# Kernel tuning notes

Measured on AMD Instinct MI355X. Metric: run time of the kernel, lower is better.

## Reference

```python
import jax, jax.numpy as jnp
import numpy as np
import math

B, S, D = 2, 2048, 2048
H, KVH, WIN = 16, 4, 256
HD = D // H            # 128
QPER = H // KVH        # 4


def setup_inputs() -> dict:
    key = jax.random.key(0)
    ks = jax.random.split(key, 9)
    s = lambda k, shp: jax.random.normal(k, shp, dtype=jnp.float32) * 0.02
    return {
        "x": jax.random.normal(ks[0], (B, S, D), dtype=jnp.float32),
        "Wq": s(ks[1], (D, D)),            "bq": jnp.zeros((D,), jnp.float32),
        "Wk": s(ks[2], (D, KVH * HD)),      "bk": jnp.zeros((KVH * HD,), jnp.float32),
        "Wv": s(ks[3], (D, KVH * HD)),      "bv": jnp.zeros((KVH * HD,), jnp.float32),
        "Wo": s(ks[4], (D, D)),            "bo": jnp.zeros((D,), jnp.float32),
    }


def reference(x, Wq, bq, Wk, bk, Wv, bv, Wo, bo):
    b, s, _ = x.shape
    # projections
    Q = (x @ Wq + bq).reshape(b, s, H, HD).transpose(0, 2, 1, 3)     # [b,H,s,hd]
    K = (x @ Wk + bk).reshape(b, s, KVH, HD).transpose(0, 2, 1, 3)   # [b,kvh,s,hd]
    V = (x @ Wv + bv).reshape(b, s, KVH, HD).transpose(0, 2, 1, 3)   # [b,kvh,s,hd]
    # GQA grouping: head h = g*QPER + q
    Qg = Q.reshape(b, KVH, QPER, s, HD)                               # [b,g,q,s,hd]
    scores = jnp.einsum('bgqsd,bgtd->bgqst', Qg, K)                   # [b,g,q,s,s]
    i = jnp.arange(s)[:, None]
    j = jnp.arange(s)[None, :]
    keep = (j <= i) & (j >= i - WIN + 1)                              # [s,s]
    scores = jnp.where(keep, scores, -jnp.inf)
    A = jax.nn.softmax(scores / math.sqrt(HD), axis=-1)
    O = jnp.einsum('bgqst,bgtd->bgqsd', A, V)                         # [b,g,q,s,hd]
    O = O.reshape(b, H, s, HD).transpose(0, 2, 1, 3).reshape(b, s, D)
    return O @ Wo + bo
```

## Files before the change

### kernel.cpp

```cpp
#include <hip/hip_runtime.h>
#include <hip/hip_bf16.h>
#include <math.h>

typedef __bf16 bf16_t;
typedef bf16_t bf16x8 __attribute__((ext_vector_type(8)));
typedef bf16_t bf16x4 __attribute__((ext_vector_type(4)));
typedef float  f32x4  __attribute__((ext_vector_type(4)));

#define NB    2
#define SEQ   2048
#define DIM   2048
#define NHEAD 16
#define NKVH  4
#define HDIM  128
#define WINSZ 256
#define KVD   512
#define QKVN  3072
#define MROWS 4096

__device__ __forceinline__ void async_copy16(const void* g, void* lds) {
    __builtin_amdgcn_global_load_lds(
        (const __attribute__((address_space(1))) void*)g,
        (__attribute__((address_space(3))) void*)lds,
        16, 0, 0);
}

__global__ __launch_bounds__(256) void cvt_f32_bf16(const float* __restrict__ in,
                                                    bf16_t* __restrict__ out, int n) {
    int i = (blockIdx.x * 256 + threadIdx.x) * 4;
    if (i >= n) return;
    float4 v = *(const float4*)(in + i);
    bf16x4 o;
    o[0] = (bf16_t)v.x; o[1] = (bf16_t)v.y; o[2] = (bf16_t)v.z; o[3] = (bf16_t)v.w;
    *(bf16x4*)(out + i) = o;
}

__global__ __launch_bounds__(256) void transpose_cvt(const float* __restrict__ in,
                                                     bf16_t* __restrict__ out, int K, int N) {
    __shared__ float tile[32][33];
    int tx = threadIdx.x & 31, ty = threadIdx.x >> 5;
    int n0 = blockIdx.x * 32, k0 = blockIdx.y * 32;
    for (int r = ty; r < 32; r += 8)
        tile[r][tx] = in[(size_t)(k0 + r) * N + n0 + tx];
    __syncthreads();
    for (int r = ty; r < 32; r += 8)
        out[(size_t)(n0 + r) * K + k0 + tx] = (bf16_t)tile[tx][r];
}

__global__ __launch_bounds__(256) void concat_bias(const float* __restrict__ bq,
                                                   const float* __restrict__ bk,
                                                   const float* __restrict__ bv,
                                                   float* __restrict__ out) {
    int i = blockIdx.x * 256 + threadIdx.x;
    if (i >= QKVN) return;
    float v = (i < DIM) ? bq[i] : ((i < DIM + KVD) ? bk[i - DIM] : bv[i - DIM - KVD]);
    out[i] = v;
}

__global__ __launch_bounds__(256) void transpose_v(const bf16_t* __restrict__ QKV,
                                                   bf16_t* __restrict__ Vtb) {
    __shared__ bf16_t t[32][33];
    int tx = threadIdx.x & 31, ty = threadIdx.x >> 5;
    int jb = blockIdx.x, c0 = blockIdx.y * 32, b = blockIdx.z;
    int j0 = jb * 32;
    for (int r = ty; r < 32; r += 8)
        t[r][tx] = QKV[((size_t)(b * SEQ) + j0 + r) * QKVN + (DIM + KVD) + c0 + tx];
    __syncthreads();
    int g = c0 >> 7, dl = c0 & 127;
    bf16_t* outb = Vtb + (((size_t)(b * NKVH) + g) * 64 + jb) * 4096;
    for (int r = ty; r < 32; r += 8)
        outb[(dl + r) * 32 + tx] = t[tx][r];
}

template <int BM, int BN, typename OutT>
__global__ __launch_bounds__(512, 1) void gemm8p(const bf16_t* __restrict__ A,
                                                 const bf16_t* __restrict__ Bt,
                                                 const float* __restrict__ bias,
                                                 OutT* __restrict__ C,
                                                 int M, int N, int K, float qs, int qcols) {
    constexpr int AISS = BM / 128;
    constexpr int BISS = BN / 128;
    constexpr int ISS  = AISS + BISS;
    constexpr int MF   = BM / 32;
    constexpr int NF   = BN / 64;
    constexpr int AHALF = BM * 32;
    constexpr int BHALF = BN * 32;
    constexpr int BUFSZ = 2 * (AHALF + BHALF);
    __shared__ bf16_t lds[2 * BUFSZ];

    const int tid  = threadIdx.x;
    const int wave = tid >> 6;
    const int lane = tid & 63;
    const int lg = lane >> 4, lc = lane & 15;
    const int wr = wave >> 2, wc = wave & 3;

    const int nbn  = N / BN;
    const int nblk = (M / BM) * nbn;
    const int qq   = nblk >> 3;
    const int swz  = (blockIdx.x & 7) * qq + (blockIdx.x >> 3);
    const long brow = (long)(swz / nbn) * BM;
    const long bcol = (long)(swz % nbn) * BN;

    const int srow   = tid >> 2;
    const int schunk = (tid & 3) ^ ((tid >> 3) & 3);

    f32x4 acc[MF][NF] = {};

    auto stage = [&](int buf, int p, int kt) {
        const int kcol = kt * 64 + p * 32 + schunk * 8;
        const bf16_t* gA = A + (brow + srow) * (long)K + kcol;
        bf16_t* dA = lds + buf * BUFSZ + p * AHALF + tid * 8;
#pragma unroll
        for (int i = 0; i < AISS; ++i)
            async_copy16(gA + (long)i * 128 * K, dA + i * 4096);
        const bf16_t* gB = Bt + (bcol + srow) * (long)K + kcol;
        bf16_t* dB = lds + buf * BUFSZ + 2 * AHALF + p * BHALF + tid * 8;
#pragma unroll
        for (int i = 0; i < BISS; ++i)
            async_copy16(gB + (long)i * 128 * K, dB + i * 4096);
    };

    stage(0, 0, 0);
    stage(0, 1, 0);

    const int NT = K >> 6;
    const int cswz = (lg ^ ((lc >> 1) & 3)) * 8;
    for (int t = 0; t < NT; ++t) {
#pragma unroll
        for (int p = 0; p < 2; ++p) {
            if (t == NT - 1 && p == 1) {
                asm volatile("s_waitcnt vmcnt(0)" ::: "memory");
            } else if constexpr (ISS == 4) {
                asm volatile("s_waitcnt vmcnt(4)" ::: "memory");
            } else {
                asm volatile("s_waitcnt vmcnt(3)" ::: "memory");
            }
            __builtin_amdgcn_s_barrier();
            asm volatile("" ::: "memory");
            const bf16_t* Ab = lds + (t & 1) * BUFSZ + p * AHALF;
            const bf16_t* Bb = lds + (t & 1) * BUFSZ + 2 * AHALF + p * BHALF;
            bf16x8 af[MF], bv[NF];
#pragma unroll
            for (int m = 0; m < MF; ++m)
                af[m] = *(const bf16x8*)(Ab + (wr * (BM / 2) + m * 16 + lc) * 32 + cswz);
#pragma unroll
            for (int n = 0; n < NF; ++n)
                bv[n] = *(const bf16x8*)(Bb + (wc * 64 + n * 16 + lc) * 32 + cswz);
            if (t + 1 < NT) stage((t + 1) & 1, p, t + 1);
            asm volatile("s_waitcnt lgkmcnt(0)" ::: "memory");
            __builtin_amdgcn_sched_barrier(0);
            __builtin_amdgcn_s_setprio(1);
#pragma unroll
            for (int m = 0; m < MF; ++m)
#pragma unroll
                for (int n = 0; n < NF; ++n)
                    acc[m][n] = __builtin_amdgcn_mfma_f32_16x16x32_bf16(af[m], bv[n], acc[m][n], 0, 0, 0);
            __builtin_amdgcn_s_setprio(0);
        }
    }

#pragma unroll
    for (int n = 0; n < NF; ++n) {
        int gc = (int)bcol + wc * 64 + n * 16 + lc;
        float bvs = bias[gc];
        bool ds = gc < qcols;
#pragma unroll
        for (int m = 0; m < MF; ++m) {
            long gr = brow + wr * (BM / 2) + m * 16 + 4 * lg;
#pragma unroll
            for (int r = 0; r < 4; ++r) {
                float v = acc[m][n][r] + bvs;
                if (ds) v *= qs;
                C[(gr + r) * (long)N + gc] = (OutT)v;
            }
        }
    }
}

__global__ __launch_bounds__(256) void attn_kernel(const bf16_t* __restrict__ QKV,
                                                   const bf16_t* __restrict__ Vtb,
                                                   bf16_t* __restrict__ Ob) {
    __shared__ bf16_t Kls[2][32 * 128];
    __shared__ bf16_t Vls[2][128 * 32];
    __shared__ bf16_t Pls[4][16 * 40];

    const int wv   = threadIdx.x >> 6;
    const int lane = threadIdx.x & 63;
    const int lg = lane >> 4, lc = lane & 15;

    const int swb = (blockIdx.x & 7) * 128 + (blockIdx.x >> 3);
    const int ti = swb & 127;
    const int g  = (swb >> 7) & 3;
    const int b  = swb >> 9;
    const int h  = g * 4 + wv;
    const int i0 = ti * 16;
    const int irow = i0 + lc;
    bf16_t* P = &Pls[wv][0];

    bf16x8 qf[4];
    {
        const bf16_t* qp = QKV + ((size_t)(b * SEQ) + irow) * QKVN + h * HDIM + lg * 8;
#pragma unroll
        for (int kk = 0; kk < 4; ++kk) qf[kk] = *(const bf16x8*)(qp + kk * 32);
    }

    auto stage = [&](int buf, int jb) {
        const int j0s = jb * 32;
        const bf16_t* kgb = QKV + ((size_t)(b * SEQ) + j0s) * QKVN + DIM + g * HDIM;
#pragma unroll
        for (int ii = 0; ii < 2; ++ii) {
            int i = wv * 2 + ii;
            int row = i * 4 + (lane >> 4);
            int ch  = (lane & 15) ^ (row & 7);
            async_copy16(kgb + (size_t)row * QKVN + ch * 8, &Kls[buf][i * 512]);
        }
        const bf16_t* vgb = Vtb + (((size_t)(b * NKVH) + g) * 64 + jb) * 4096;
#pragma unroll
        for (int ii = 0; ii < 2; ++ii) {
            int i = wv * 2 + ii;
            int row = i * 16 + (lane >> 2);
            int ch  = (lane & 3) ^ ((row ^ (row >> 2)) & 3);
            async_copy16(vgb + row * 32 + ch * 8, &Vls[buf][i * 512]);
        }
    };

    float m_run = -1e30f, l_run = 0.f;
    f32x4 oacc[8] = {};

    int jlo = i0 - (WINSZ - 1); if (jlo < 0) jlo = 0;
    const int jb0 = jlo >> 5;
    const int jb1 = (i0 + 15) >> 5;

    stage(0, jb0);

    for (int jb = jb0; jb <= jb1; ++jb) {
        const int j0 = jb * 32;
        const int cur = (jb - jb0) & 1;
        asm volatile("s_waitcnt vmcnt(0)" ::: "memory");
        __builtin_amdgcn_s_barrier();
        asm volatile("" ::: "memory");

        bf16x8 kf[2][4];
#pragma unroll
        for (int t = 0; t < 2; ++t)
#pragma unroll
            for (int kk = 0; kk < 4; ++kk) {
                int row = t * 16 + lc;
                int ch  = (kk * 4 + lg) ^ (row & 7);
                kf[t][kk] = *(const bf16x8*)(&Kls[cur][row * 128 + ch * 8]);
            }
        if (jb < jb1) stage(cur ^ 1, jb + 1);
        asm volatile("s_waitcnt lgkmcnt(0)" ::: "memory");
        __builtin_amdgcn_sched_barrier(0);

        f32x4 s[2];
        __builtin_amdgcn_s_setprio(1);
#pragma unroll
        for (int t = 0; t < 2; ++t) {
            f32x4 sv = {};
#pragma unroll
            for (int kk = 0; kk < 4; ++kk)
                sv = __builtin_amdgcn_mfma_f32_16x16x32_bf16(kf[t][kk], qf[kk], sv, 0, 0, 0);
            s[t] = sv;
        }
        __builtin_amdgcn_s_setprio(0);

        const bool edge = (j0 < i0 - 240) || (j0 > i0 - 31);
        if (edge) {
#pragma unroll
            for (int t = 0; t < 2; ++t)
#pragma unroll
                for (int r = 0; r < 4; ++r) {
                    int j = j0 + t * 16 + 4 * lg + r;
                    if (j > irow || j < irow - (WINSZ - 1)) s[t][r] = -1e30f;
                }
        }
        float tmax = fmaxf(fmaxf(fmaxf(s[0][0], s[0][1]), fmaxf(s[0][2], s[0][3])),
                           fmaxf(fmaxf(s[1][0], s[1][1]), fmaxf(s[1][2], s[1][3])));
        tmax = fmaxf(tmax, __shfl_xor(tmax, 16, 64));
        tmax = fmaxf(tmax, __shfl_xor(tmax, 32, 64));
        if (!__all(tmax - m_run <= 8.0f)) {
            float m_new = fmaxf(m_run, tmax);
            float resc = __builtin_amdgcn_exp2f(m_run - m_new);
            l_run *= resc;
#pragma unroll
            for (int c = 0; c < 8; ++c) {
                oacc[c][0] *= resc; oacc[c][1] *= resc;
                oacc[c][2] *= resc; oacc[c][3] *= resc;
            }
            m_run = m_new;
        }
        float psum = 0.f;
#pragma unroll
        for (int t = 0; t < 2; ++t) {
            bf16x4 pk;
#pragma unroll
            for (int r = 0; r < 4; ++r) {
                float sv = s[t][r];
                float p = (edge && sv < -5e29f) ? 0.f : __builtin_amdgcn_exp2f(sv - m_run);
                psum += p;
                pk[r] = (bf16_t)p;
            }
            *(bf16x4*)(P + lc * 40 + t * 16 + lg * 4) = pk;
        }
        psum += __shfl_xor(psum, 16, 64);
        psum += __shfl_xor(psum, 32, 64);
        l_run += psum;
        asm volatile("" ::: "memory");

        bf16x8 vf[8];
#pragma unroll
        for (int c = 0; c < 8; ++c) {
            int row = c * 16 + lc;
            int ch  = lg ^ ((row ^ (row >> 2)) & 3);
            vf[c] = *(const bf16x8*)(&Vls[cur][row * 32 + ch * 8]);
        }
        bf16x8 pf = *(const bf16x8*)(P + lc * 40 + lg * 8);

        __builtin_amdgcn_s_setprio(1);
#pragma unroll
        for (int c = 0; c < 8; ++c)
            oacc[c] = __builtin_amdgcn_mfma_f32_16x16x32_bf16(vf[c], pf, oacc[c], 0, 0, 0);
        __builtin_amdgcn_s_setprio(0);
    }

    const float inv = 1.f / l_run;
#pragma unroll
    for (int c = 0; c < 8; ++c) {
        bf16x4 ov;
#pragma unroll
        for (int r = 0; r < 4; ++r) ov[r] = (bf16_t)(oacc[c][r] * inv);
        *(bf16x4*)(Ob + ((size_t)(b * SEQ) + irow) * DIM + h * HDIM + c * 16 + lg * 4) = ov;
    }
}

extern "C" void kernel_launch(void* const* d_in, const int* in_sizes, int n_in,
                              void* d_out, int out_size, void* d_ws, size_t ws_size,
                              hipStream_t stream) {
    const float* x  = (const float*)d_in[0];
    const float* Wq = (const float*)d_in[1];
    const float* bq = (const float*)d_in[2];
    const float* Wk = (const float*)d_in[3];
    const float* bk = (const float*)d_in[4];
    const float* Wv = (const float*)d_in[5];
    const float* bv = (const float*)d_in[6];
    const float* Wo = (const float*)d_in[7];
    const float* bo = (const float*)d_in[8];
    float* out = (float*)d_out;

    char* ws = (char*)d_ws;
    bf16_t* xb    = (bf16_t*)(ws);
    bf16_t* WqkvT = (bf16_t*)(ws + (16u << 20));
    bf16_t* WoT   = (bf16_t*)(ws + (28u << 20));
    bf16_t* QKVb  = (bf16_t*)(ws + (36u << 20));
    float*  bqkv  = (float*) (ws + (60u << 20));
    bf16_t* Vtb   = WqkvT;
    bf16_t* Ob    = xb;

    const float qs = 0.12751707498038074f;

    cvt_f32_bf16<<<(MROWS * DIM) / 1024, 256, 0, stream>>>(x, xb, MROWS * DIM);
    transpose_cvt<<<dim3(DIM / 32, DIM / 32), 256, 0, stream>>>(Wq, WqkvT, DIM, DIM);
    transpose_cvt<<<dim3(KVD / 32, DIM / 32), 256, 0, stream>>>(Wk, WqkvT + (size_t)DIM * DIM, DIM, KVD);
    transpose_cvt<<<dim3(KVD / 32, DIM / 32), 256, 0, stream>>>(Wv, WqkvT + (size_t)(DIM + KVD) * DIM, DIM, KVD);
    transpose_cvt<<<dim3(DIM / 32, DIM / 32), 256, 0, stream>>>(Wo, WoT, DIM, DIM);
    concat_bias<<<(QKVN + 255) / 256, 256, 0, stream>>>(bq, bk, bv, bqkv);

    gemm8p<256, 256, bf16_t><<<dim3((MROWS / 256) * (QKVN / 256)), 512, 0, stream>>>(
        xb, WqkvT, bqkv, QKVb, MROWS, QKVN, DIM, qs, DIM);

    transpose_v<<<dim3(SEQ / 32, KVD / 32, NB), 256, 0, stream>>>(QKVb, Vtb);

    attn_kernel<<<dim3(NB * NKVH * (SEQ / 16)), 256, 0, stream>>>(QKVb, Vtb, Ob);

    gemm8p<128, 256, float><<<dim3((MROWS / 128) * (DIM / 256)), 512, 0, stream>>>(
        Ob, WoT, bo, out, MROWS, DIM, DIM, 1.0f, 0);
}
```

Before: 159.9 us.

## Restructure GEMM pipelines with finer-grained async staging and triple buffering

Replaces the templated double-buffered GEMM with two specialised kernels. The 256x256 QKV kernel splits each k-tile into four A/B quarter stages issued at different sub-steps, prefetching two tiles ahead. The 128x256 output-projection kernel uses a three-stage LDS ring, also prefetching two tiles ahead. Both aim to hide global-load latency better behind MFMA work, at the cost of more LDS, extra barriers and trickier vmcnt bookkeeping that could cause races if the counts are wrong.

```diff
diff --git a/kernel.cpp b/kernel.cpp
--- a/kernel.cpp
+++ b/kernel.cpp
@@ -72,101 +72,197 @@
         outb[(dl + r) * 32 + tx] = t[tx][r];
 }
 
-template <int BM, int BN, typename OutT>
-__global__ __launch_bounds__(512, 1) void gemm8p(const bf16_t* __restrict__ A,
-                                                 const bf16_t* __restrict__ Bt,
-                                                 const float* __restrict__ bias,
-                                                 OutT* __restrict__ C,
-                                                 int M, int N, int K, float qs, int qcols) {
-    constexpr int AISS = BM / 128;
-    constexpr int BISS = BN / 128;
-    constexpr int ISS  = AISS + BISS;
-    constexpr int MF   = BM / 32;
-    constexpr int NF   = BN / 64;
-    constexpr int AHALF = BM * 32;
-    constexpr int BHALF = BN * 32;
-    constexpr int BUFSZ = 2 * (AHALF + BHALF);
-    __shared__ bf16_t lds[2 * BUFSZ];
-
-    const int tid  = threadIdx.x;
-    const int wave = tid >> 6;
-    const int lane = tid & 63;
+template <typename OutT>
+__global__ __launch_bounds__(512, 1) void gemm_v8(const bf16_t* __restrict__ A,
+                                                  const bf16_t* __restrict__ Bt,
+                                                  const float* __restrict__ bias,
+                                                  OutT* __restrict__ C,
+                                                  int M, int N, int K, float qs, int qcols) {
+    __shared__ bf16_t lds[2][32768];
+    const int tid = threadIdx.x, wave = tid >> 6, lane = tid & 63;
     const int lg = lane >> 4, lc = lane & 15;
     const int wr = wave >> 2, wc = wave & 3;
-
-    const int nbn  = N / BN;
-    const int nblk = (M / BM) * nbn;
-    const int qq   = nblk >> 3;
-    const int swz  = (blockIdx.x & 7) * qq + (blockIdx.x >> 3);
-    const long brow = (long)(swz / nbn) * BM;
-    const long bcol = (long)(swz % nbn) * BN;
-
-    const int srow   = tid >> 2;
-    const int schunk = (tid & 3) ^ ((tid >> 3) & 3);
-
-    f32x4 acc[MF][NF] = {};
-
-    auto stage = [&](int buf, int p, int kt) {
-        const int kcol = kt * 64 + p * 32 + schunk * 8;
-        const bf16_t* gA = A + (brow + srow) * (long)K + kcol;
-        bf16_t* dA = lds + buf * BUFSZ + p * AHALF + tid * 8;
-#pragma unroll
-        for (int i = 0; i < AISS; ++i)
-            async_copy16(gA + (long)i * 128 * K, dA + i * 4096);
-        const bf16_t* gB = Bt + (bcol + srow) * (long)K + kcol;
-        bf16_t* dB = lds + buf * BUFSZ + 2 * AHALF + p * BHALF + tid * 8;
-#pragma unroll
-        for (int i = 0; i < BISS; ++i)
-            async_copy16(gB + (long)i * 128 * K, dB + i * 4096);
+    const int nbn = N >> 8, nblk = (M >> 8) * nbn, qq = nblk >> 3;
+    const int swz = (blockIdx.x & 7) * qq + (blockIdx.x >> 3);
+    const long brow = (long)(swz / nbn) << 8;
+    const long bcol = (long)(swz % nbn) << 8;
+    const int rl = tid >> 2, cd = tid & 3;
+    const int csw = (lg ^ ((lc >> 1) & 3)) * 8;
+
+    f32x4 acc[8][4] = {};
+
+    auto stgA = [&](int bf, int kt, int ks) {
+#pragma unroll
+        for (int h = 0; h < 2; ++h) {
+            int row = h * 128 + rl;
+            int sc = cd ^ ((row >> 1) & 3);
+            async_copy16(A + (brow + row) * (long)K + kt * 64 + ks * 32 + sc * 8,
+                         &lds[bf][ks * 8192 + h * 4096 + wave * 512]);
+        }
     };
-
-    stage(0, 0, 0);
-    stage(0, 1, 0);
+    auto stgB = [&](int bf, int kt, int ks) {
+#pragma unroll
+        for (int h = 0; h < 2; ++h) {
+            int row = h * 128 + rl;
+            int sc = cd ^ ((row >> 1) & 3);
+            async_copy16(Bt + (bcol + row) * (long)K + kt * 64 + ks * 32 + sc * 8,
+                         &lds[bf][16384 + ks * 8192 + h * 4096 + wave * 512]);
+        }
+    };
 
     const int NT = K >> 6;
-    const int cswz = (lg ^ ((lc >> 1) & 3)) * 8;
+    stgA(0, 0, 0); stgA(0, 0, 1); stgB(0, 0, 0); stgB(0, 0, 1);
+    stgA(1, 1, 0); stgB(1, 1, 0); stgB(1, 1, 1);
+    asm volatile("s_waitcnt vmcnt(0)" ::: "memory");
+    __builtin_amdgcn_s_barrier();
+    asm volatile("" ::: "memory");
+
+    bf16x8 bv[4];
     for (int t = 0; t < NT; ++t) {
-#pragma unroll
-        for (int p = 0; p < 2; ++p) {
-            if (t == NT - 1 && p == 1) {
-                asm volatile("s_waitcnt vmcnt(0)" ::: "memory");
-            } else if constexpr (ISS == 4) {
-                asm volatile("s_waitcnt vmcnt(4)" ::: "memory");
-            } else {
-                asm volatile("s_waitcnt vmcnt(3)" ::: "memory");
-            }
+        const int bf = t & 1;
+#pragma unroll
+        for (int p = 0; p < 4; ++p) {
+            const int ks = p >> 1, mh = p & 1;
+            bf16x8 af[4];
+#pragma unroll
+            for (int m = 0; m < 4; ++m) {
+                int row = wr * 128 + (mh * 4 + m) * 16 + lc;
+                af[m] = *(const bf16x8*)&lds[bf][ks * 8192 + row * 32 + csw];
+            }
+            if (mh == 0) {
+#pragma unroll
+                for (int n = 0; n < 4; ++n) {
+                    int row = wc * 64 + n * 16 + lc;
+                    bv[n] = *(const bf16x8*)&lds[bf][16384 + ks * 8192 + row * 32 + csw];
+                }
+            }
+            if (p == 0)      { if (t + 1 < NT) stgA(bf ^ 1, t + 1, 1); }
+            else if (p == 1) { if (t + 2 < NT) stgB(bf, t + 2, 0); }
+            else if (p == 2) { if (t + 2 < NT) stgA(bf, t + 2, 0); }
+            else             { if (t + 2 < NT) stgB(bf, t + 2, 1); }
             __builtin_amdgcn_s_barrier();
-            asm volatile("" ::: "memory");
-            const bf16_t* Ab = lds + (t & 1) * BUFSZ + p * AHALF;
-            const bf16_t* Bb = lds + (t & 1) * BUFSZ + 2 * AHALF + p * BHALF;
-            bf16x8 af[MF], bv[NF];
-#pragma unroll
-            for (int m = 0; m < MF; ++m)
-                af[m] = *(const bf16x8*)(Ab + (wr * (BM / 2) + m * 16 + lc) * 32 + cswz);
-#pragma unroll
-            for (int n = 0; n < NF; ++n)
-                bv[n] = *(const bf16x8*)(Bb + (wc * 64 + n * 16 + lc) * 32 + cswz);
-            if (t + 1 < NT) stage((t + 1) & 1, p, t + 1);
             asm volatile("s_waitcnt lgkmcnt(0)" ::: "memory");
             __builtin_amdgcn_sched_barrier(0);
             __builtin_amdgcn_s_setprio(1);
 #pragma unroll
-            for (int m = 0; m < MF; ++m)
-#pragma unroll
-                for (int n = 0; n < NF; ++n)
-                    acc[m][n] = __builtin_amdgcn_mfma_f32_16x16x32_bf16(af[m], bv[n], acc[m][n], 0, 0, 0);
+            for (int m = 0; m < 4; ++m)
+#pragma unroll
+                for (int n = 0; n < 4; ++n)
+                    acc[mh * 4 + m][n] =
+                        __builtin_amdgcn_mfma_f32_16x16x32_bf16(af[m], bv[n], acc[mh * 4 + m][n], 0, 0, 0);
             __builtin_amdgcn_s_setprio(0);
-        }
-    }
-
-#pragma unroll
-    for (int n = 0; n < NF; ++n) {
+            if (t >= NT - 3) asm volatile("s_waitcnt vmcnt(0)" ::: "memory");
+            else             asm volatile("s_waitcnt vmcnt(4)" ::: "memory");
+            __builtin_amdgcn_s_barrier();
+            asm volatile("" ::: "memory");
+        }
+    }
+
+#pragma unroll
+    for (int n = 0; n < 4; ++n) {
         int gc = (int)bcol + wc * 64 + n * 16 + lc;
         float bvs = bias[gc];
         bool ds = gc < qcols;
 #pragma unroll
-        for (int m = 0; m < MF; ++m) {
-            long gr = brow + wr * (BM / 2) + m * 16 + 4 * lg;
+        for (int m = 0; m < 8; ++m) {
+            long gr = brow + wr * 128 + m * 16 + 4 * lg;
+#pragma unroll
+            for (int r = 0; r < 4; ++r) {
+                float v = acc[m][n][r] + bvs;
+                if (ds) v *= qs;
+                C[(gr + r) * (long)N + gc] = (OutT)v;
+            }
+        }
+    }
+}
+
+template <typename OutT>
+__global__ __launch_bounds__(512, 1) void gemm_v2(const bf16_t* __restrict__ A,
+                                                  const bf16_t* __restrict__ Bt,
+                                                  const float* __restrict__ bias,
+                                                  OutT* __restrict__ C,
+                                                  int M, int N, int K, float qs, int qcols) {
+    __shared__ bf16_t lds[3][24576];
+    const int tid = threadIdx.x, wave = tid >> 6, lane = tid & 63;
+    const int lg = lane >> 4, lc = lane & 15;
+    const int wr = wave >> 2, wc = wave & 3;
+    const int nbn = N >> 8, nblk = (M >> 7) * nbn, qq = nblk >> 3;
+    const int swz = (blockIdx.x & 7) * qq + (blockIdx.x >> 3);
+    const long brow = (long)(swz / nbn) << 7;
+    const long bcol = (long)(swz % nbn) << 8;
+    const int rl = tid >> 2, cd = tid & 3;
+    const int csw = (lg ^ ((lc >> 1) & 3)) * 8;
+
+    f32x4 acc[4][4] = {};
+
+    auto stg = [&](int bf, int kt, int ks) {
+        {
+            int row = rl;
+            int sc = cd ^ ((row >> 1) & 3);
+            async_copy16(A + (brow + row) * (long)K + kt * 64 + ks * 32 + sc * 8,
+                         &lds[bf][ks * 4096 + wave * 512]);
+        }
+#pragma unroll
+        for (int h = 0; h < 2; ++h) {
+            int row = h * 128 + rl;
+            int sc = cd ^ ((row >> 1) & 3);
+            async_copy16(Bt + (bcol + row) * (long)K + kt * 64 + ks * 32 + sc * 8,
+                         &lds[bf][8192 + ks * 8192 + h * 4096 + wave * 512]);
+        }
+    };
+
+    const int NT = K >> 6;
+    stg(0, 0, 0); stg(0, 0, 1);
+    stg(1, 1, 0); stg(1, 1, 1);
+    asm volatile("s_waitcnt vmcnt(0)" ::: "memory");
+    __builtin_amdgcn_s_barrier();
+    asm volatile("" ::: "memory");
+
+    for (int t = 0; t < NT; ++t) {
+        const int bf = t % 3;
+        const int b2 = (t + 2) % 3;
+#pragma unroll
+        for (int p = 0; p < 2; ++p) {
+            const int ks = p;
+            bf16x8 af[4], bv[4];
+#pragma unroll
+            for (int m = 0; m < 4; ++m) {
+                int row = wr * 64 + m * 16 + lc;
+                af[m] = *(const bf16x8*)&lds[bf][ks * 4096 + row * 32 + csw];
+            }
+#pragma unroll
+            for (int n = 0; n < 4; ++n) {
+                int row = wc * 64 + n * 16 + lc;
+                bv[n] = *(const bf16x8*)&lds[bf][8192 + ks * 8192 + row * 32 + csw];
+            }
+            if (t + 2 < NT) stg(b2, t + 2, p);
+            __builtin_amdgcn_s_barrier();
+            asm volatile("s_waitcnt lgkmcnt(0)" ::: "memory");
+            __builtin_amdgcn_sched_barrier(0);
+            __builtin_amdgcn_s_setprio(1);
+#pragma unroll
+            for (int m = 0; m < 4; ++m)
+#pragma unroll
+                for (int n = 0; n < 4; ++n)
+                    acc[m][n] = __builtin_amdgcn_mfma_f32_16x16x32_bf16(af[m], bv[n], acc[m][n], 0, 0, 0);
+            __builtin_amdgcn_s_setprio(0);
+            if (p == 1) {
+                if (t >= NT - 3) asm volatile("s_waitcnt vmcnt(0)" ::: "memory");
+                else             asm volatile("s_waitcnt vmcnt(6)" ::: "memory");
+            }
+            __builtin_amdgcn_s_barrier();
+            asm volatile("" ::: "memory");
+        }
+    }
+
+#pragma unroll
+    for (int n = 0; n < 4; ++n) {
+        int gc = (int)bcol + wc * 64 + n * 16 + lc;
+        float bvs = bias[gc];
+        bool ds = gc < qcols;
+#pragma unroll
+        for (int m = 0; m < 4; ++m) {
+            long gr = brow + wr * 64 + m * 16 + 4 * lg;
 #pragma unroll
             for (int r = 0; r < 4; ++r) {
                 float v = acc[m][n][r] + bvs;
@@ -366,13 +462,13 @@
     transpose_cvt<<<dim3(DIM / 32, DIM / 32), 256, 0, stream>>>(Wo, WoT, DIM, DIM);
     concat_bias<<<(QKVN + 255) / 256, 256, 0, stream>>>(bq, bk, bv, bqkv);
 
-    gemm8p<256, 256, bf16_t><<<dim3((MROWS / 256) * (QKVN / 256)), 512, 0, stream>>>(
+    gemm_v8<bf16_t><<<dim3((MROWS / 256) * (QKVN / 256)), 512, 0, stream>>>(
         xb, WqkvT, bqkv, QKVb, MROWS, QKVN, DIM, qs, DIM);
 
     transpose_v<<<dim3(SEQ / 32, KVD / 32, NB), 256, 0, stream>>>(QKVb, Vtb);
 
     attn_kernel<<<dim3(NB * NKVH * (SEQ / 16)), 256, 0, stream>>>(QKVb, Vtb, Ob);
 
-    gemm8p<128, 256, float><<<dim3((MROWS / 128) * (DIM / 256)), 512, 0, stream>>>(
+    gemm_v2<float><<<dim3((MROWS / 128) * (DIM / 256)), 512, 0, stream>>>(
         Ob, WoT, bo, out, MROWS, DIM, DIM, 1.0f, 0);
 }
```

Result: slower. 171.1 us (+7.0%).
